# Optimization experiments

Hardware: AMD Instinct MI355X
Metric: run time of the kernel (lower is better)

## Reference

```python
import jax, jax.numpy as jnp
import numpy as np

HIDDEN = 1024
INTER = 1408
N_EXPERTS = 8
TOP_K = 2
BATCH, SEQ = 2, 1024


def setup_inputs() -> dict:
    key = jax.random.key(0)
    k1, k2, k3, k4, k5 = jax.random.split(key, 5)
    scale_in = 1.0 / np.sqrt(HIDDEN)
    scale_mid = 1.0 / np.sqrt(INTER)
    return {
        "hidden_states": jax.random.normal(k1, (BATCH, SEQ, HIDDEN), dtype=jnp.float32),
        # router: torch Linear(hidden, n_experts, bias=False) -> weight [E, hidden]
        "router_w": jax.random.normal(k2, (N_EXPERTS, HIDDEN), dtype=jnp.float32) * scale_in,
        # per-expert SwiGLU MLP weights, stored pre-transposed for x @ W
        "wg": jax.random.normal(k3, (N_EXPERTS, HIDDEN, INTER), dtype=jnp.float32) * scale_in,
        "wu": jax.random.normal(k4, (N_EXPERTS, HIDDEN, INTER), dtype=jnp.float32) * scale_in,
        "wd": jax.random.normal(k5, (N_EXPERTS, INTER, HIDDEN), dtype=jnp.float32) * scale_mid,
    }


def reference(hidden_states, router_w, wg, wu, wd):
    B, S, D = hidden_states.shape
    x = hidden_states.reshape(-1, D)  # [T, D]
    T = x.shape[0]
    E = router_w.shape[0]

    # Router: softmax over experts in float32, then top-k and renormalize (norm_topk_prob=True)
    logits = x @ router_w.T  # [T, E]
    probs = jax.nn.softmax(logits.astype(jnp.float32), axis=-1)
    topk_w, topk_idx = jax.lax.top_k(probs, TOP_K)  # [T, K]
    topk_w = topk_w / jnp.sum(topk_w, axis=-1, keepdims=True)
    topk_w = topk_w.astype(x.dtype)

    # Dense combine weights [T, E]: zero for unrouted experts -> math-identical to sparse dispatch
    combine = jnp.zeros((T, E), dtype=x.dtype).at[
        jnp.arange(T)[:, None], topk_idx
    ].add(topk_w)

    # Expert SwiGLU MLPs computed as batched GEMMs over experts
    g = jnp.einsum('td,edf->etf', x, wg)  # [E, T, INTER]
    u = jnp.einsum('td,edf->etf', x, wu)
    h = jax.nn.silu(g) * u
    y = jnp.einsum('etf,efd->etd', h, wd)  # [E, T, D]

    out = jnp.einsum('etd,te->td', y, combine)  # weighted combine
    return out.reshape(B, S, D)
```

## Files before the change

### kernel.cpp

```cpp
#include <hip/hip_runtime.h>
#include <math.h>

#define HIDDEN 1024
#define INTER  1408
#define NEXP   8
#define NTOK   2048
#define KSPLIT_LEN 704

typedef short s16x8 __attribute__((ext_vector_type(8)));
typedef float f32x4 __attribute__((ext_vector_type(4)));

static __device__ __forceinline__ short f2b(float f) {
  union { float f; unsigned u; } v; v.f = f;
  unsigned u = v.u;
  unsigned r = (u + 0x7FFFu + ((u >> 16) & 1u)) >> 16;
  return (short)r;
}

__global__ __launch_bounds__(256) void router_choice(
    const float* __restrict__ x, const float* __restrict__ rw,
    int* __restrict__ ce, float2* __restrict__ cw, short* __restrict__ xb)
{
  int wave = threadIdx.x >> 6;
  int lane = threadIdx.x & 63;
  int t = blockIdx.x * 4 + wave;
  if (t >= NTOK) return;
  const float* xt = x + (size_t)t * HIDDEN;
  float xr[16];
#pragma unroll
  for (int i = 0; i < 16; ++i) xr[i] = xt[lane + 64 * i];

  short* xo = xb + (size_t)t * HIDDEN;
#pragma unroll
  for (int i = 0; i < 16; ++i) xo[lane + 64 * i] = f2b(xr[i]);

  float logits[NEXP];
#pragma unroll
  for (int e = 0; e < NEXP; ++e) {
    const float* w = rw + e * HIDDEN;
    float acc = 0.f;
#pragma unroll
    for (int i = 0; i < 16; ++i) acc = fmaf(xr[i], w[lane + 64 * i], acc);
#pragma unroll
    for (int off = 32; off > 0; off >>= 1) acc += __shfl_xor(acc, off);
    logits[e] = acc;
  }
  if (lane == 0) {
    float mx = logits[0];
#pragma unroll
    for (int e = 1; e < NEXP; ++e) mx = fmaxf(mx, logits[e]);
    float p[NEXP];
#pragma unroll
    for (int e = 0; e < NEXP; ++e) p[e] = expf(logits[e] - mx);
    int i0 = 0;
#pragma unroll
    for (int e = 1; e < NEXP; ++e) if (p[e] > p[i0]) i0 = e;
    int i1 = (i0 == 0) ? 1 : 0;
#pragma unroll
    for (int e = 0; e < NEXP; ++e) { if (e != i0 && p[e] > p[i1]) i1 = e; }
    float denom = p[i0] + p[i1];
    ce[t] = i0 | (i1 << 8);
    cw[t] = make_float2(p[i0] / denom, p[i1] / denom);
  }
}

__global__ __launch_bounds__(256) void build_lists(
    const int* __restrict__ ce, const float2* __restrict__ cw,
    int* __restrict__ counts, int* __restrict__ base,
    int* __restrict__ tok_list, float* __restrict__ w_list)
{
  int e = blockIdx.x;
  int tid = threadIdx.x;
  __shared__ int hall[256][8];
  __shared__ int hsum[8];
  __shared__ int scan[256];

  int cloc[8];
  int h[8] = {0,0,0,0,0,0,0,0};
  int myc = 0;
#pragma unroll
  for (int j = 0; j < 8; ++j) {
    int c = ce[tid * 8 + j];
    cloc[j] = c;
    int e0 = c & 255, e1 = (c >> 8) & 255;
    h[e0]++; h[e1]++;
    myc += (e0 == e) + (e1 == e);
  }
#pragma unroll
  for (int k = 0; k < 8; ++k) hall[tid][k] = h[k];
  scan[tid] = myc;
  __syncthreads();

  if (tid < 8) {
    int s = 0;
    for (int i = 0; i < 256; ++i) s += hall[i][tid];
    hsum[tid] = s;
  }
  int v = myc;
  for (int off = 1; off < 256; off <<= 1) {
    int prev = (tid >= off) ? scan[tid - off] : 0;
    __syncthreads();
    v = v + prev;
    scan[tid] = v;
    __syncthreads();
  }
  int pos = v - myc;

  if (tid == 0) {
    int b = 0;
    for (int k = 0; k < e; ++k) b += hsum[k];
    base[e] = b;
    counts[e] = hsum[e];
  }

#pragma unroll
  for (int j = 0; j < 8; ++j) {
    int t = tid * 8 + j;
    int c = cloc[j];
    int e0 = c & 255, e1 = (c >> 8) & 255;
    if (e0 == e) {
      float2 w = cw[t];
      tok_list[e * NTOK + pos] = t;
      w_list[e * NTOK + pos] = w.x;
      pos++;
    } else if (e1 == e) {
      float2 w = cw[t];
      tok_list[e * NTOK + pos] = t | (1 << 16);
      w_list[e * NTOK + pos] = w.y;
      pos++;
    }
  }
}

__global__ __launch_bounds__(256) void wconv(
    const float* __restrict__ wg, const float* __restrict__ wu,
    const float* __restrict__ wd,
    short* __restrict__ wgT, short* __restrict__ wuT, short* __restrict__ wdT)
{
  int id = blockIdx.x;
  int wave = threadIdx.x >> 6;
  int lane = threadIdx.x & 63;
  int mat = id / 1408;
  int r = id - mat * 1408;
  int e = r / 176;
  int t = r - e * 176;

  const float* src; short* dst; int K, N;
  if (mat == 0)      { src = wg; dst = wgT; K = HIDDEN; N = INTER; }
  else if (mat == 1) { src = wu; dst = wuT; K = HIDDEN; N = INTER; }
  else               { src = wd; dst = wdT; K = INTER;  N = HIDDEN; }

  int nstr = N >> 6;
  int ks = t / nstr, nt = t - ks * nstr;
  int n0 = nt * 64;
  int k0 = ks * 128 + wave * 32;

  const float* se = src + (size_t)e * (HIDDEN * INTER);
  short*       de = dst + (size_t)e * (HIDDEN * INTER);
  int n = n0 + lane;

  float v[32];
#pragma unroll
  for (int j = 0; j < 32; ++j) v[j] = se[(size_t)(k0 + j) * N + n];

  unsigned pk[16];
#pragma unroll
  for (int j = 0; j < 16; ++j) {
    unsigned lo = (unsigned short)f2b(v[2 * j]);
    unsigned hi = (unsigned short)f2b(v[2 * j + 1]);
    pk[j] = lo | (hi << 16);
  }

  short* dp = de + (size_t)n * K + k0;
#pragma unroll
  for (int c = 0; c < 4; ++c) {
    uint4 o = make_uint4(pk[4 * c], pk[4 * c + 1], pk[4 * c + 2], pk[4 * c + 3]);
    *(uint4*)(dp + 8 * c) = o;
  }
}


__global__ __launch_bounds__(256, 2) void gateup_mfma(
    const short* __restrict__ xb, const short* __restrict__ wgT,
    const short* __restrict__ wuT,
    const int* __restrict__ counts, const int* __restrict__ base,
    const int* __restrict__ tok_list, short* __restrict__ hbuf)
{
  int id = blockIdx.x;
  int xcd = id & 7;
  int rest = id >> 3;
  int mslot = rest & 15;
  int g = (rest >> 4) * 8 + xcd;
  int e = g / 11;
  int n0 = (g - e * 11) * 128;
  int cnt = counts[e];
  int m0 = mslot * 128;
  if (m0 >= cnt) return;

  __shared__ short As[128 * 32];
  __shared__ short Bg[128 * 32];
  __shared__ short Bu[128 * 32];
  __shared__ int toks[128];

  int tid = threadIdx.x;
  if (tid < 128) {
    int r = m0 + tid;
    toks[tid] = tok_list[e * NTOK + (r < cnt ? r : cnt - 1)] & 0xFFFF;
  }
  __syncthreads();

  int sr = tid >> 1;
  int h = tid & 1;
  int key = (sr >> 1) & 3;
  int pair = ((2 * h) ^ key) >> 1;
  int sw = (key & 1) * 8;
  const short* gA = xb + (size_t)toks[sr] * HIDDEN + pair * 16;
  const short* gG = wgT + ((size_t)e * INTER + n0 + sr) * HIDDEN + pair * 16;
  const short* gU = wuT + ((size_t)e * INTER + n0 + sr) * HIDDEN + pair * 16;
  short* wA0 = &As[sr * 32 + h * 16 + sw];
  short* wA1 = &As[sr * 32 + h * 16 + (8 - sw)];
  short* wG0 = &Bg[sr * 32 + h * 16 + sw];
  short* wG1 = &Bg[sr * 32 + h * 16 + (8 - sw)];
  short* wU0 = &Bu[sr * 32 + h * 16 + sw];
  short* wU1 = &Bu[sr * 32 + h * 16 + (8 - sw)];

  int wv = tid >> 6, lane = tid & 63;
  int wm = wv & 1, wn = wv >> 1;
  int q = lane >> 4, ml = lane & 15;
  int chk = q ^ ((ml >> 1) & 3);
  const short* ard = &As[(wm * 64 + ml) * 32 + chk * 8];
  const short* grd = &Bg[(wn * 64 + ml) * 32 + chk * 8];
  const short* urd = &Bu[(wn * 64 + ml) * 32 + chk * 8];

  f32x4 accg[4][4], accu[4][4];
#pragma unroll
  for (int i = 0; i < 4; ++i)
#pragma unroll
    for (int j = 0; j < 4; ++j) { accg[i][j] = (f32x4)0.f; accu[i][j] = (f32x4)0.f; }

  s16x8 a0 = *(const s16x8*)(gA);     s16x8 a1 = *(const s16x8*)(gA + 8);
  s16x8 g0 = *(const s16x8*)(gG);     s16x8 g1 = *(const s16x8*)(gG + 8);
  s16x8 u0 = *(const s16x8*)(gU);     s16x8 u1 = *(const s16x8*)(gU + 8);

  for (int k0 = 0; k0 < HIDDEN; k0 += 32) {
    __syncthreads();
    *(s16x8*)wA0 = a0; *(s16x8*)wA1 = a1;
    *(s16x8*)wG0 = g0; *(s16x8*)wG1 = g1;
    *(s16x8*)wU0 = u0; *(s16x8*)wU1 = u1;
    __syncthreads();

    int kn = (k0 + 32) & (HIDDEN - 1);
    a0 = *(const s16x8*)(gA + kn);     a1 = *(const s16x8*)(gA + kn + 8);
    g0 = *(const s16x8*)(gG + kn);     g1 = *(const s16x8*)(gG + kn + 8);
    u0 = *(const s16x8*)(gU + kn);     u1 = *(const s16x8*)(gU + kn + 8);

    s16x8 af[4], gf[4], uf[4];
#pragma unroll
    for (int i = 0; i < 4; ++i) af[i] = *(const s16x8*)(ard + i * 16 * 32);
#pragma unroll
    for (int j = 0; j < 4; ++j) {
      gf[j] = *(const s16x8*)(grd + j * 16 * 32);
      uf[j] = *(const s16x8*)(urd + j * 16 * 32);
    }
#pragma unroll
    for (int i = 0; i < 4; ++i)
#pragma unroll
      for (int j = 0; j < 4; ++j) {
        accg[i][j] = __builtin_amdgcn_mfma_f32_16x16x32_bf16(af[i], gf[j], accg[i][j], 0, 0, 0);
        accu[i][j] = __builtin_amdgcn_mfma_f32_16x16x32_bf16(af[i], uf[j], accu[i][j], 0, 0, 0);
      }
  }

  int hb = base[e];
#pragma unroll
  for (int i = 0; i < 4; ++i)
#pragma unroll
    for (int ii = 0; ii < 4; ++ii) {
      int r = m0 + wm * 64 + i * 16 + q * 4 + ii;
      if (r < cnt) {
        short* hp = hbuf + (size_t)(hb + r) * INTER + n0 + wn * 64 + ml;
#pragma unroll
        for (int j = 0; j < 4; ++j) {
          float gg = accg[i][j][ii], uu = accu[i][j][ii];
          float hh = (gg / (1.f + __expf(-gg))) * uu;
          hp[j * 16] = f2b(hh);
        }
      }
    }
}

__global__ __launch_bounds__(256, 3) void down_mfma(
    const short* __restrict__ hbuf, const short* __restrict__ wdT,
    const int* __restrict__ counts, const int* __restrict__ base,
    const int* __restrict__ tok_list, const float* __restrict__ w_list,
    float* __restrict__ ybuf)
{
  int id = blockIdx.x;
  int xcd = id & 7;
  int rest = id >> 3;
  int mslot = rest & 15;
  int g = (rest >> 4) * 8 + xcd;
  int e = g >> 4;
  int ks = (g >> 3) & 1;
  int n0 = (g & 7) * 128;
  int cnt = counts[e];
  int m0 = mslot * 128;
  if (m0 >= cnt) return;

  __shared__ short As[128 * 32];
  __shared__ short Bs[128 * 32];

  int tid = threadIdx.x;
  int hb = base[e];
  int kbeg = ks * KSPLIT_LEN, kend = kbeg + KSPLIT_LEN;

  int sr = tid >> 1;
  int h = tid & 1;
  int key = (sr >> 1) & 3;
  int pair = ((2 * h) ^ key) >> 1;
  int sw = (key & 1) * 8;
  int ra = m0 + sr; if (ra >= cnt) ra = cnt - 1;
  const short* gA = hbuf + (size_t)(hb + ra) * INTER + pair * 16;
  const short* gB = wdT + ((size_t)e * HIDDEN + n0 + sr) * INTER + pair * 16;
  short* wA0 = &As[sr * 32 + h * 16 + sw];
  short* wA1 = &As[sr * 32 + h * 16 + (8 - sw)];
  short* wB0 = &Bs[sr * 32 + h * 16 + sw];
  short* wB1 = &Bs[sr * 32 + h * 16 + (8 - sw)];

  int wv = tid >> 6, lane = tid & 63;
  int wm = wv & 1, wn = wv >> 1;
  int q = lane >> 4, ml = lane & 15;
  int chk = q ^ ((ml >> 1) & 3);
  const short* ard = &As[(wm * 64 + ml) * 32 + chk * 8];
  const short* brd = &Bs[(wn * 64 + ml) * 32 + chk * 8];

  f32x4 acc[4][4];
#pragma unroll
  for (int i = 0; i < 4; ++i)
#pragma unroll
    for (int j = 0; j < 4; ++j) acc[i][j] = (f32x4)0.f;

  s16x8 a0 = *(const s16x8*)(gA + kbeg);  s16x8 a1 = *(const s16x8*)(gA + kbeg + 8);
  s16x8 b0 = *(const s16x8*)(gB + kbeg);  s16x8 b1 = *(const s16x8*)(gB + kbeg + 8);

  for (int k0 = kbeg; k0 < kend; k0 += 32) {
    __syncthreads();
    *(s16x8*)wA0 = a0; *(s16x8*)wA1 = a1;
    *(s16x8*)wB0 = b0; *(s16x8*)wB1 = b1;
    __syncthreads();

    int kn = k0 + 32; if (kn >= kend) kn = kbeg;
    a0 = *(const s16x8*)(gA + kn);  a1 = *(const s16x8*)(gA + kn + 8);
    b0 = *(const s16x8*)(gB + kn);  b1 = *(const s16x8*)(gB + kn + 8);

    s16x8 af[4], bf[4];
#pragma unroll
    for (int i = 0; i < 4; ++i) af[i] = *(const s16x8*)(ard + i * 16 * 32);
#pragma unroll
    for (int j = 0; j < 4; ++j) bf[j] = *(const s16x8*)(brd + j * 16 * 32);
#pragma unroll
    for (int i = 0; i < 4; ++i)
#pragma unroll
      for (int j = 0; j < 4; ++j)
        acc[i][j] = __builtin_amdgcn_mfma_f32_16x16x32_bf16(af[i], bf[j], acc[i][j], 0, 0, 0);
  }

#pragma unroll
  for (int i = 0; i < 4; ++i)
#pragma unroll
    for (int ii = 0; ii < 4; ++ii) {
      int r = m0 + wm * 64 + i * 16 + q * 4 + ii;
      if (r < cnt) {
        int ent = tok_list[e * NTOK + r];
        int tok = ent & 0xFFFF, slot = ent >> 16;
        float wgt = w_list[e * NTOK + r];
        float* yp = ybuf + ((size_t)(slot * 2 + ks) * NTOK + tok) * HIDDEN
                    + n0 + wn * 64 + ml;
#pragma unroll
        for (int j = 0; j < 4; ++j)
          yp[j * 16] = acc[i][j][ii] * wgt;
      }
    }
}

__global__ __launch_bounds__(256) void combine_kernel(
    const float* __restrict__ ybuf, float* __restrict__ out)
{
  size_t i = (size_t)blockIdx.x * 256 + threadIdx.x;
  const size_t S = (size_t)NTOK * HIDDEN / 4;
  float4 a = ((const float4*)ybuf)[i];
  float4 b = ((const float4*)ybuf)[i + S];
  float4 c = ((const float4*)ybuf)[i + 2 * S];
  float4 d = ((const float4*)ybuf)[i + 3 * S];
  float4 o;
  o.x = (a.x + b.x) + (c.x + d.x);
  o.y = (a.y + b.y) + (c.y + d.y);
  o.z = (a.z + b.z) + (c.z + d.z);
  o.w = (a.w + b.w) + (c.w + d.w);
  ((float4*)out)[i] = o;
}

extern "C" void kernel_launch(void* const* d_in, const int* in_sizes, int n_in,
                              void* d_out, int out_size, void* d_ws, size_t ws_size,
                              hipStream_t stream)
{
  const float* x  = (const float*)d_in[0];
  const float* rw = (const float*)d_in[1];
  const float* wg = (const float*)d_in[2];
  const float* wu = (const float*)d_in[3];
  const float* wd = (const float*)d_in[4];
  float* out = (float*)d_out;

  char* ws = (char*)d_ws;
  int*    counts   = (int*)(ws);
  int*    base     = (int*)(ws + 32);
  int*    tok_list = (int*)(ws + 64);
  float*  w_list   = (float*)(ws + 64 + NEXP * NTOK * 4);
  size_t off = 64 + 2 * (size_t)NEXP * NTOK * 4;
  int*    ce = (int*)(ws + off);     off += NTOK * 4;
  float2* cw = (float2*)(ws + off);  off += NTOK * 8;
  short* xb  = (short*)(ws + off);  off += (size_t)NTOK * HIDDEN * 2;
  short* wgT = (short*)(ws + off);  off += (size_t)NEXP * HIDDEN * INTER * 2;
  short* wuT = (short*)(ws + off);  off += (size_t)NEXP * HIDDEN * INTER * 2;
  short* wdT = (short*)(ws + off);  off += (size_t)NEXP * HIDDEN * INTER * 2;
  short* hbuf = (short*)(ws + off);
  float* ybuf = (float*)wgT;

  router_choice<<<NTOK / 4, 256, 0, stream>>>(x, rw, ce, cw, xb);
  build_lists<<<NEXP, 256, 0, stream>>>(ce, cw, counts, base, tok_list, w_list);

  wconv<<<3 * NEXP * 176, 256, 0, stream>>>(wg, wu, wd, wgT, wuT, wdT);

  gateup_mfma<<<8 * 16 * 11, 256, 0, stream>>>(xb, wgT, wuT, counts, base, tok_list, hbuf);
  down_mfma<<<8 * 16 * 16, 256, 0, stream>>>(hbuf, wdT, counts, base, tok_list, w_list, ybuf);

  combine_kernel<<<(NTOK * HIDDEN / 4) / 256, 256, 0, stream>>>(ybuf, out);
}
```

Before: 287.4 us.

## Store converted bf16 weights in K-chunked [K/8][N][8] layout for coalesced writes

The weight conversion kernel now writes bf16 weights as 8-element K chunks interleaved across N, so adjacent lanes write adjacent 16-byte chunks instead of strided rows. Each wave handles one 32xK by 64xN tile. The gate/up and down GEMM kernels are updated to read B tiles from this new layout using per-k-block offsets. This is meant to cut the uncoalesced-store cost of the transpose-conversion pass, at the price of more scattered B-tile loads in the GEMMs (16-byte chunks with an INTER*8 or HIDDEN*8 stride).

Result: faster. 269.8 us (-6.1%).

```diff
diff --git a/kernel.cpp b/kernel.cpp
--- a/kernel.cpp
+++ b/kernel.cpp
@@ -16,6 +16,7 @@
   unsigned r = (u + 0x7FFFu + ((u >> 16) & 1u)) >> 16;
   return (short)r;
 }
+
 
 __global__ __launch_bounds__(256) void router_choice(
     const float* __restrict__ x, const float* __restrict__ rw,
@@ -137,45 +138,40 @@
     const float* __restrict__ wd,
     short* __restrict__ wgT, short* __restrict__ wuT, short* __restrict__ wdT)
 {
-  int id = blockIdx.x;
-  int wave = threadIdx.x >> 6;
+  int gw = blockIdx.x * 4 + (threadIdx.x >> 6);
   int lane = threadIdx.x & 63;
-  int mat = id / 1408;
-  int r = id - mat * 1408;
-  int e = r / 176;
-  int t = r - e * 176;
-
-  const float* src; short* dst; int K, N;
-  if (mat == 0)      { src = wg; dst = wgT; K = HIDDEN; N = INTER; }
-  else if (mat == 1) { src = wu; dst = wuT; K = HIDDEN; N = INTER; }
-  else               { src = wd; dst = wdT; K = INTER;  N = HIDDEN; }
-
-  int nstr = N >> 6;
-  int ks = t / nstr, nt = t - ks * nstr;
-  int n0 = nt * 64;
-  int k0 = ks * 128 + wave * 32;
-
-  const float* se = src + (size_t)e * (HIDDEN * INTER);
-  short*       de = dst + (size_t)e * (HIDDEN * INTER);
-  int n = n0 + lane;
+  int mat = gw / 5632;
+  int r = gw - mat * 5632;
+  int e = r / 704;
+  int t = r - e * 704;
+
+  const float* src; short* dst; int N, nstr;
+  if (mat == 0)      { src = wg; dst = wgT; N = INTER;  nstr = 22; }
+  else if (mat == 1) { src = wu; dst = wuT; N = INTER;  nstr = 22; }
+  else               { src = wd; dst = wdT; N = HIDDEN; nstr = 16; }
+
+  int kb = t / nstr, nt = t - kb * nstr;
+  int n = nt * 64 + lane;
+
+  const float* se = src + (size_t)e * (HIDDEN * INTER)
+                        + (size_t)(kb * 32) * N + n;
+  short* de = dst + (size_t)e * (HIDDEN * INTER);
 
   float v[32];
 #pragma unroll
-  for (int j = 0; j < 32; ++j) v[j] = se[(size_t)(k0 + j) * N + n];
-
-  unsigned pk[16];
-#pragma unroll
-  for (int j = 0; j < 16; ++j) {
-    unsigned lo = (unsigned short)f2b(v[2 * j]);
-    unsigned hi = (unsigned short)f2b(v[2 * j + 1]);
-    pk[j] = lo | (hi << 16);
-  }
-
-  short* dp = de + (size_t)n * K + k0;
-#pragma unroll
-  for (int c = 0; c < 4; ++c) {
-    uint4 o = make_uint4(pk[4 * c], pk[4 * c + 1], pk[4 * c + 2], pk[4 * c + 3]);
-    *(uint4*)(dp + 8 * c) = o;
+  for (int j = 0; j < 32; ++j) v[j] = se[(size_t)j * N];
+
+#pragma unroll
+  for (int kc = 0; kc < 4; ++kc) {
+    unsigned pk[4];
+#pragma unroll
+    for (int m = 0; m < 4; ++m) {
+      unsigned lo = (unsigned short)f2b(v[8 * kc + 2 * m]);
+      unsigned hi = (unsigned short)f2b(v[8 * kc + 2 * m + 1]);
+      pk[m] = lo | (hi << 16);
+    }
+    *(uint4*)(de + ((size_t)(kb * 4 + kc) * N + n) * 8) =
+        make_uint4(pk[0], pk[1], pk[2], pk[3]);
   }
 }
 
@@ -215,8 +211,10 @@
   int pair = ((2 * h) ^ key) >> 1;
   int sw = (key & 1) * 8;
   const short* gA = xb + (size_t)toks[sr] * HIDDEN + pair * 16;
-  const short* gG = wgT + ((size_t)e * INTER + n0 + sr) * HIDDEN + pair * 16;
-  const short* gU = wuT + ((size_t)e * INTER + n0 + sr) * HIDDEN + pair * 16;
+  size_t ebase = (size_t)e * (HIDDEN * INTER);
+  size_t boff = (size_t)(2 * pair) * (INTER * 8) + (size_t)(n0 + sr) * 8;
+  const short* gGb = wgT + ebase + boff;
+  const short* gUb = wuT + ebase + boff;
   short* wA0 = &As[sr * 32 + h * 16 + sw];
   short* wA1 = &As[sr * 32 + h * 16 + (8 - sw)];
   short* wG0 = &Bg[sr * 32 + h * 16 + sw];
@@ -239,8 +237,8 @@
     for (int j = 0; j < 4; ++j) { accg[i][j] = (f32x4)0.f; accu[i][j] = (f32x4)0.f; }
 
   s16x8 a0 = *(const s16x8*)(gA);     s16x8 a1 = *(const s16x8*)(gA + 8);
-  s16x8 g0 = *(const s16x8*)(gG);     s16x8 g1 = *(const s16x8*)(gG + 8);
-  s16x8 u0 = *(const s16x8*)(gU);     s16x8 u1 = *(const s16x8*)(gU + 8);
+  s16x8 g0 = *(const s16x8*)(gGb);    s16x8 g1 = *(const s16x8*)(gGb + INTER * 8);
+  s16x8 u0 = *(const s16x8*)(gUb);    s16x8 u1 = *(const s16x8*)(gUb + INTER * 8);
 
   for (int k0 = 0; k0 < HIDDEN; k0 += 32) {
     __syncthreads();
@@ -250,9 +248,10 @@
     __syncthreads();
 
     int kn = (k0 + 32) & (HIDDEN - 1);
-    a0 = *(const s16x8*)(gA + kn);     a1 = *(const s16x8*)(gA + kn + 8);
-    g0 = *(const s16x8*)(gG + kn);     g1 = *(const s16x8*)(gG + kn + 8);
-    u0 = *(const s16x8*)(gU + kn);     u1 = *(const s16x8*)(gU + kn + 8);
+    size_t kboff = (size_t)(kn >> 5) * (4 * INTER * 8);
+    a0 = *(const s16x8*)(gA + kn);         a1 = *(const s16x8*)(gA + kn + 8);
+    g0 = *(const s16x8*)(gGb + kboff);     g1 = *(const s16x8*)(gGb + kboff + INTER * 8);
+    u0 = *(const s16x8*)(gUb + kboff);     u1 = *(const s16x8*)(gUb + kboff + INTER * 8);
 
     s16x8 af[4], gf[4], uf[4];
 #pragma unroll
@@ -321,7 +320,9 @@
   int sw = (key & 1) * 8;
   int ra = m0 + sr; if (ra >= cnt) ra = cnt - 1;
   const short* gA = hbuf + (size_t)(hb + ra) * INTER + pair * 16;
-  const short* gB = wdT + ((size_t)e * HIDDEN + n0 + sr) * INTER + pair * 16;
+  size_t ebase = (size_t)e * (HIDDEN * INTER);
+  const short* gBb = wdT + ebase + (size_t)(2 * pair) * (HIDDEN * 8)
+                         + (size_t)(n0 + sr) * 8;
   short* wA0 = &As[sr * 32 + h * 16 + sw];
   short* wA1 = &As[sr * 32 + h * 16 + (8 - sw)];
   short* wB0 = &Bs[sr * 32 + h * 16 + sw];
@@ -340,8 +341,10 @@
 #pragma unroll
     for (int j = 0; j < 4; ++j) acc[i][j] = (f32x4)0.f;
 
+  size_t kboff0 = (size_t)(kbeg >> 5) * (4 * HIDDEN * 8);
   s16x8 a0 = *(const s16x8*)(gA + kbeg);  s16x8 a1 = *(const s16x8*)(gA + kbeg + 8);
-  s16x8 b0 = *(const s16x8*)(gB + kbeg);  s16x8 b1 = *(const s16x8*)(gB + kbeg + 8);
+  s16x8 b0 = *(const s16x8*)(gBb + kboff0);
+  s16x8 b1 = *(const s16x8*)(gBb + kboff0 + HIDDEN * 8);
 
   for (int k0 = kbeg; k0 < kend; k0 += 32) {
     __syncthreads();
@@ -350,8 +353,10 @@
     __syncthreads();
 
     int kn = k0 + 32; if (kn >= kend) kn = kbeg;
+    size_t kboff = (size_t)(kn >> 5) * (4 * HIDDEN * 8);
     a0 = *(const s16x8*)(gA + kn);  a1 = *(const s16x8*)(gA + kn + 8);
-    b0 = *(const s16x8*)(gB + kn);  b1 = *(const s16x8*)(gB + kn + 8);
+    b0 = *(const s16x8*)(gBb + kboff);
+    b1 = *(const s16x8*)(gBb + kboff + HIDDEN * 8);
 
     s16x8 af[4], bf[4];
 #pragma unroll
@@ -429,7 +434,7 @@
   router_choice<<<NTOK / 4, 256, 0, stream>>>(x, rw, ce, cw, xb);
   build_lists<<<NEXP, 256, 0, stream>>>(ce, cw, counts, base, tok_list, w_list);
 
-  wconv<<<3 * NEXP * 176, 256, 0, stream>>>(wg, wu, wd, wgT, wuT, wdT);
+  wconv<<<4224, 256, 0, stream>>>(wg, wu, wd, wgT, wuT, wdT);
 
   gateup_mfma<<<8 * 16 * 11, 256, 0, stream>>>(xb, wgT, wuT, counts, base, tok_list, hbuf);
   down_mfma<<<8 * 16 * 16, 256, 0, stream>>>(hbuf, wdT, counts, base, tok_list, w_list, ybuf);
```

## Fuse fp32 weight conversion into MoE GEMM B-tile staging, drop wconv pass

Applied to the files above, without the earlier changes.

Removes the separate weight transpose/convert kernel and has the gate/up and down GEMMs read the fp32 expert weights directly. Each thread loads float4 rows, converts pairs to bf16, and exchanges halves across the wave with shuffles so the shared-memory tile keeps its K-major layout. This avoids writing and re-reading about 69 MB of bf16 transposed weights per call. The cost is twice the bytes per B-tile load in the GEMM main loops, repeated across the token M-tiles, plus extra conversion and shuffle work inside the loop.

After: 319.5 us. 11.2% more time.

```diff
diff --git a/kernel.cpp b/kernel.cpp
--- a/kernel.cpp
+++ b/kernel.cpp
@@ -1,4 +1,5 @@
 #include <hip/hip_runtime.h>
+#include <hip/hip_bf16.h>
 #include <math.h>
 
 #define HIDDEN 1024
@@ -15,6 +16,39 @@
   unsigned u = v.u;
   unsigned r = (u + 0x7FFFu + ((u >> 16) & 1u)) >> 16;
   return (short)r;
+}
+
+static __device__ __forceinline__ unsigned cvtpk2(float a, float b) {
+  __hip_bfloat162 h = __float22bfloat162_rn(make_float2(a, b));
+  union { __hip_bfloat162 h; unsigned u; } v; v.h = h;
+  return v.u;
+}
+
+static __device__ __forceinline__ void stage_b_fp32(
+    const float* __restrict__ p, int stride, int hb2,
+    uint4& c0, uint4& c1)
+{
+  float4 t0 = *(const float4*)(p);
+  float4 t1 = *(const float4*)(p + stride);
+  float4 t2 = *(const float4*)(p + 2 * (size_t)stride);
+  float4 t3 = *(const float4*)(p + 3 * (size_t)stride);
+  unsigned p0 = cvtpk2(t0.x, t1.x), p1 = cvtpk2(t2.x, t3.x);
+  unsigned p2 = cvtpk2(t0.y, t1.y), p3 = cvtpk2(t2.y, t3.y);
+  unsigned p4 = cvtpk2(t0.z, t1.z), p5 = cvtpk2(t2.z, t3.z);
+  unsigned p6 = cvtpk2(t0.w, t1.w), p7 = cvtpk2(t2.w, t3.w);
+  unsigned s0 = hb2 ? p0 : p4, s1 = hb2 ? p1 : p5;
+  unsigned s2 = hb2 ? p2 : p6, s3 = hb2 ? p3 : p7;
+  unsigned r0 = (unsigned)__shfl_xor((int)s0, 32);
+  unsigned r1 = (unsigned)__shfl_xor((int)s1, 32);
+  unsigned r2 = (unsigned)__shfl_xor((int)s2, 32);
+  unsigned r3 = (unsigned)__shfl_xor((int)s3, 32);
+  if (hb2 == 0) {
+    c0 = make_uint4(p0, p1, r0, r1);
+    c1 = make_uint4(p2, p3, r2, r3);
+  } else {
+    c0 = make_uint4(r0, r1, p4, p5);
+    c1 = make_uint4(r2, r3, p6, p7);
+  }
 }
 
 __global__ __launch_bounds__(256) void router_choice(
@@ -132,57 +166,9 @@
   }
 }
 
-__global__ __launch_bounds__(256) void wconv(
-    const float* __restrict__ wg, const float* __restrict__ wu,
-    const float* __restrict__ wd,
-    short* __restrict__ wgT, short* __restrict__ wuT, short* __restrict__ wdT)
-{
-  int id = blockIdx.x;
-  int wave = threadIdx.x >> 6;
-  int lane = threadIdx.x & 63;
-  int mat = id / 1408;
-  int r = id - mat * 1408;
-  int e = r / 176;
-  int t = r - e * 176;
-
-  const float* src; short* dst; int K, N;
-  if (mat == 0)      { src = wg; dst = wgT; K = HIDDEN; N = INTER; }
-  else if (mat == 1) { src = wu; dst = wuT; K = HIDDEN; N = INTER; }
-  else               { src = wd; dst = wdT; K = INTER;  N = HIDDEN; }
-
-  int nstr = N >> 6;
-  int ks = t / nstr, nt = t - ks * nstr;
-  int n0 = nt * 64;
-  int k0 = ks * 128 + wave * 32;
-
-  const float* se = src + (size_t)e * (HIDDEN * INTER);
-  short*       de = dst + (size_t)e * (HIDDEN * INTER);
-  int n = n0 + lane;
-
-  float v[32];
-#pragma unroll
-  for (int j = 0; j < 32; ++j) v[j] = se[(size_t)(k0 + j) * N + n];
-
-  unsigned pk[16];
-#pragma unroll
-  for (int j = 0; j < 16; ++j) {
-    unsigned lo = (unsigned short)f2b(v[2 * j]);
-    unsigned hi = (unsigned short)f2b(v[2 * j + 1]);
-    pk[j] = lo | (hi << 16);
-  }
-
-  short* dp = de + (size_t)n * K + k0;
-#pragma unroll
-  for (int c = 0; c < 4; ++c) {
-    uint4 o = make_uint4(pk[4 * c], pk[4 * c + 1], pk[4 * c + 2], pk[4 * c + 3]);
-    *(uint4*)(dp + 8 * c) = o;
-  }
-}
-
-
 __global__ __launch_bounds__(256, 2) void gateup_mfma(
-    const short* __restrict__ xb, const short* __restrict__ wgT,
-    const short* __restrict__ wuT,
+    const short* __restrict__ xb, const float* __restrict__ wg,
+    const float* __restrict__ wu,
     const int* __restrict__ counts, const int* __restrict__ base,
     const int* __restrict__ tok_list, short* __restrict__ hbuf)
 {
@@ -209,22 +195,27 @@
   }
   __syncthreads();
 
-  int sr = tid >> 1;
-  int h = tid & 1;
+  int sr = tid >> 1, ha = tid & 1;
   int key = (sr >> 1) & 3;
-  int pair = ((2 * h) ^ key) >> 1;
+  int pair = ((2 * ha) ^ key) >> 1;
   int sw = (key & 1) * 8;
   const short* gA = xb + (size_t)toks[sr] * HIDDEN + pair * 16;
-  const short* gG = wgT + ((size_t)e * INTER + n0 + sr) * HIDDEN + pair * 16;
-  const short* gU = wuT + ((size_t)e * INTER + n0 + sr) * HIDDEN + pair * 16;
-  short* wA0 = &As[sr * 32 + h * 16 + sw];
-  short* wA1 = &As[sr * 32 + h * 16 + (8 - sw)];
-  short* wG0 = &Bg[sr * 32 + h * 16 + sw];
-  short* wG1 = &Bg[sr * 32 + h * 16 + (8 - sw)];
-  short* wU0 = &Bu[sr * 32 + h * 16 + sw];
-  short* wU1 = &Bu[sr * 32 + h * 16 + (8 - sw)];
+  short* wA0 = &As[sr * 32 + ha * 16 + sw];
+  short* wA1 = &As[sr * 32 + ha * 16 + (8 - sw)];
 
   int wv = tid >> 6, lane = tid & 63;
+  int li = lane & 31, hb2 = lane >> 5;
+  size_t wbase = (size_t)e * (HIDDEN * INTER)
+               + (size_t)(8 * wv + 4 * hb2) * INTER + n0 + 4 * li;
+  const float* gG = wg + wbase;
+  const float* gU = wu + wbase;
+  int rn0 = 4 * li + 2 * hb2, rn1 = rn0 + 1;
+  int ph = wv ^ ((rn0 >> 1) & 3);
+  short* wG0 = &Bg[rn0 * 32 + ph * 8];
+  short* wG1 = &Bg[rn1 * 32 + ph * 8];
+  short* wU0 = &Bu[rn0 * 32 + ph * 8];
+  short* wU1 = &Bu[rn1 * 32 + ph * 8];
+
   int wm = wv & 1, wn = wv >> 1;
   int q = lane >> 4, ml = lane & 15;
   int chk = q ^ ((ml >> 1) & 3);
@@ -239,20 +230,21 @@
     for (int j = 0; j < 4; ++j) { accg[i][j] = (f32x4)0.f; accu[i][j] = (f32x4)0.f; }
 
   s16x8 a0 = *(const s16x8*)(gA);     s16x8 a1 = *(const s16x8*)(gA + 8);
-  s16x8 g0 = *(const s16x8*)(gG);     s16x8 g1 = *(const s16x8*)(gG + 8);
-  s16x8 u0 = *(const s16x8*)(gU);     s16x8 u1 = *(const s16x8*)(gU + 8);
+  uint4 g0c, g1c, u0c, u1c;
+  stage_b_fp32(gG, INTER, hb2, g0c, g1c);
+  stage_b_fp32(gU, INTER, hb2, u0c, u1c);
 
   for (int k0 = 0; k0 < HIDDEN; k0 += 32) {
     __syncthreads();
     *(s16x8*)wA0 = a0; *(s16x8*)wA1 = a1;
-    *(s16x8*)wG0 = g0; *(s16x8*)wG1 = g1;
-    *(s16x8*)wU0 = u0; *(s16x8*)wU1 = u1;
+    *(uint4*)wG0 = g0c; *(uint4*)wG1 = g1c;
+    *(uint4*)wU0 = u0c; *(uint4*)wU1 = u1c;
     __syncthreads();
 
     int kn = (k0 + 32) & (HIDDEN - 1);
-    a0 = *(const s16x8*)(gA + kn);     a1 = *(const s16x8*)(gA + kn + 8);
-    g0 = *(const s16x8*)(gG + kn);     g1 = *(const s16x8*)(gG + kn + 8);
-    u0 = *(const s16x8*)(gU + kn);     u1 = *(const s16x8*)(gU + kn + 8);
+    a0 = *(const s16x8*)(gA + kn);  a1 = *(const s16x8*)(gA + kn + 8);
+    stage_b_fp32(gG + (size_t)kn * INTER, INTER, hb2, g0c, g1c);
+    stage_b_fp32(gU + (size_t)kn * INTER, INTER, hb2, u0c, u1c);
 
     s16x8 af[4], gf[4], uf[4];
 #pragma unroll
@@ -290,7 +282,7 @@
 }
 
 __global__ __launch_bounds__(256, 3) void down_mfma(
-    const short* __restrict__ hbuf, const short* __restrict__ wdT,
+    const short* __restrict__ hbuf, const float* __restrict__ wd,
     const int* __restrict__ counts, const int* __restrict__ base,
     const int* __restrict__ tok_list, const float* __restrict__ w_list,
     float* __restrict__ ybuf)
@@ -314,20 +306,24 @@
   int hb = base[e];
   int kbeg = ks * KSPLIT_LEN, kend = kbeg + KSPLIT_LEN;
 
-  int sr = tid >> 1;
-  int h = tid & 1;
+  int sr = tid >> 1, ha = tid & 1;
   int key = (sr >> 1) & 3;
-  int pair = ((2 * h) ^ key) >> 1;
+  int pair = ((2 * ha) ^ key) >> 1;
   int sw = (key & 1) * 8;
   int ra = m0 + sr; if (ra >= cnt) ra = cnt - 1;
   const short* gA = hbuf + (size_t)(hb + ra) * INTER + pair * 16;
-  const short* gB = wdT + ((size_t)e * HIDDEN + n0 + sr) * INTER + pair * 16;
-  short* wA0 = &As[sr * 32 + h * 16 + sw];
-  short* wA1 = &As[sr * 32 + h * 16 + (8 - sw)];
-  short* wB0 = &Bs[sr * 32 + h * 16 + sw];
-  short* wB1 = &Bs[sr * 32 + h * 16 + (8 - sw)];
+  short* wA0 = &As[sr * 32 + ha * 16 + sw];
+  short* wA1 = &As[sr * 32 + ha * 16 + (8 - sw)];
 
   int wv = tid >> 6, lane = tid & 63;
+  int li = lane & 31, hb2 = lane >> 5;
+  const float* gB = wd + (size_t)e * (HIDDEN * INTER)
+                  + (size_t)(8 * wv + 4 * hb2) * HIDDEN + n0 + 4 * li;
+  int rn0 = 4 * li + 2 * hb2, rn1 = rn0 + 1;
+  int ph = wv ^ ((rn0 >> 1) & 3);
+  short* wB0 = &Bs[rn0 * 32 + ph * 8];
+  short* wB1 = &Bs[rn1 * 32 + ph * 8];
+
   int wm = wv & 1, wn = wv >> 1;
   int q = lane >> 4, ml = lane & 15;
   int chk = q ^ ((ml >> 1) & 3);
@@ -341,17 +337,18 @@
     for (int j = 0; j < 4; ++j) acc[i][j] = (f32x4)0.f;
 
   s16x8 a0 = *(const s16x8*)(gA + kbeg);  s16x8 a1 = *(const s16x8*)(gA + kbeg + 8);
-  s16x8 b0 = *(const s16x8*)(gB + kbeg);  s16x8 b1 = *(const s16x8*)(gB + kbeg + 8);
+  uint4 b0c, b1c;
+  stage_b_fp32(gB + (size_t)kbeg * HIDDEN, HIDDEN, hb2, b0c, b1c);
 
   for (int k0 = kbeg; k0 < kend; k0 += 32) {
     __syncthreads();
     *(s16x8*)wA0 = a0; *(s16x8*)wA1 = a1;
-    *(s16x8*)wB0 = b0; *(s16x8*)wB1 = b1;
+    *(uint4*)wB0 = b0c; *(uint4*)wB1 = b1c;
     __syncthreads();
 
     int kn = k0 + 32; if (kn >= kend) kn = kbeg;
     a0 = *(const s16x8*)(gA + kn);  a1 = *(const s16x8*)(gA + kn + 8);
-    b0 = *(const s16x8*)(gB + kn);  b1 = *(const s16x8*)(gB + kn + 8);
+    stage_b_fp32(gB + (size_t)kn * HIDDEN, HIDDEN, hb2, b0c, b1c);
 
     s16x8 af[4], bf[4];
 #pragma unroll
@@ -419,20 +416,15 @@
   size_t off = 64 + 2 * (size_t)NEXP * NTOK * 4;
   int*    ce = (int*)(ws + off);     off += NTOK * 4;
   float2* cw = (float2*)(ws + off);  off += NTOK * 8;
-  short* xb  = (short*)(ws + off);  off += (size_t)NTOK * HIDDEN * 2;
-  short* wgT = (short*)(ws + off);  off += (size_t)NEXP * HIDDEN * INTER * 2;
-  short* wuT = (short*)(ws + off);  off += (size_t)NEXP * HIDDEN * INTER * 2;
-  short* wdT = (short*)(ws + off);  off += (size_t)NEXP * HIDDEN * INTER * 2;
-  short* hbuf = (short*)(ws + off);
-  float* ybuf = (float*)wgT;
+  short* xb   = (short*)(ws + off);  off += (size_t)NTOK * HIDDEN * 2;
+  short* hbuf = (short*)(ws + off);  off += (size_t)2 * NTOK * INTER * 2;
+  float* ybuf = (float*)(ws + off);
 
   router_choice<<<NTOK / 4, 256, 0, stream>>>(x, rw, ce, cw, xb);
   build_lists<<<NEXP, 256, 0, stream>>>(ce, cw, counts, base, tok_list, w_list);
 
-  wconv<<<3 * NEXP * 176, 256, 0, stream>>>(wg, wu, wd, wgT, wuT, wdT);
-
-  gateup_mfma<<<8 * 16 * 11, 256, 0, stream>>>(xb, wgT, wuT, counts, base, tok_list, hbuf);
-  down_mfma<<<8 * 16 * 16, 256, 0, stream>>>(hbuf, wdT, counts, base, tok_list, w_list, ybuf);
+  gateup_mfma<<<8 * 16 * 11, 256, 0, stream>>>(xb, wg, wu, counts, base, tok_list, hbuf);
+  down_mfma<<<8 * 16 * 16, 256, 0, stream>>>(hbuf, wd, counts, base, tok_list, w_list, ybuf);
 
   combine_kernel<<<(NTOK * HIDDEN / 4) / 256, 256, 0, stream>>>(ybuf, out);
 }
```
